# Performance work log

Measured on AMD Instinct MI355X. Metric: run time of the kernel, lower is better.

Reference implementation:

```python
import jax, jax.numpy as jnp
import numpy as np

EPS = 1e-7
N_CAPS1 = 1152  # 32 maps * 6 * 6
D_CAPS1 = 8
N_CAPS2 = 10
D_CAPS2 = 16


def squash(s, axis=-1):
    sq = jnp.sum(jnp.square(s), axis=axis, keepdims=True)
    return (sq / (1.0 + sq)) * s / jnp.sqrt(sq + EPS)


def conv2d_relu(x, w, b, stride):
    y = jax.lax.conv_general_dilated(
        x, w, window_strides=(stride, stride), padding='VALID',
        dimension_numbers=('NHWC', 'HWIO', 'NHWC'))
    return jax.nn.relu(y + b)


def setup_inputs() -> dict:
    key = jax.random.key(0)
    ks = jax.random.split(key, 10)
    B = 128
    image = jax.random.normal(ks[0], (B, 28, 28, 1), dtype=jnp.float32)
    target = jax.random.randint(ks[1], (B,), 0, N_CAPS2)
    conv1_w = jax.random.normal(ks[2], (9, 9, 1, 256), dtype=jnp.float32) * 0.05
    conv1_b = jnp.zeros((256,), jnp.float32)
    conv2_w = jax.random.normal(ks[3], (9, 9, 256, 256), dtype=jnp.float32) * 0.01
    conv2_b = jnp.zeros((256,), jnp.float32)
    W = jax.random.normal(ks[4], (1, N_CAPS1, N_CAPS2, D_CAPS2, D_CAPS1), dtype=jnp.float32) * 0.1
    d1_w = jax.random.normal(ks[5], (N_CAPS2 * D_CAPS2, 512), dtype=jnp.float32) * 0.05
    d1_b = jnp.zeros((512,), jnp.float32)
    d2_w = jax.random.normal(ks[6], (512, 1024), dtype=jnp.float32) * 0.05
    d2_b = jnp.zeros((1024,), jnp.float32)
    do_w = jax.random.normal(ks[7], (1024, 28 * 28), dtype=jnp.float32) * 0.05
    do_b = jnp.zeros((28 * 28,), jnp.float32)
    return dict(image=image, target=target, conv1_w=conv1_w, conv1_b=conv1_b,
                conv2_w=conv2_w, conv2_b=conv2_b, W=W,
                d1_w=d1_w, d1_b=d1_b, d2_w=d2_w, d2_b=d2_b, do_w=do_w, do_b=do_b)


def reference(image, target, conv1_w, conv1_b, conv2_w, conv2_b, W,
              d1_w, d1_b, d2_w, d2_b, do_w, do_b):
    B = image.shape[0]
    # Convolutional feature extraction: 28x28x1 -> 20x20x256 -> 6x6x256
    x = conv2d_relu(image, conv1_w, conv1_b, 1)
    x = conv2d_relu(x, conv2_w, conv2_b, 2)
    # Primary capsules [B, 1152, 8]
    pc = squash(x.reshape(B, N_CAPS1, D_CAPS1), axis=-1)
    # Prediction vectors u_hat[b,i,j,d] (einsum replaces tile+matmul)
    u_hat = jnp.einsum('ijdk,bik->bijd', W[0], pc)[..., None]  # [B,1152,10,16,1]
    # --- dynamic routing, 2 rounds ---
    raw = jnp.zeros((B, N_CAPS1, N_CAPS2, 1, 1), jnp.float32)
    c1 = jax.nn.softmax(raw, axis=2)
    s1 = jnp.sum(c1 * u_hat, axis=1, keepdims=True)      # [B,1,10,16,1]
    v1 = squash(s1, axis=-2)
    uv1 = jnp.sum(u_hat * v1, axis=-2, keepdims=True)    # agreement [B,1152,10,1,1]
    raw = raw + uv1
    c2 = jax.nn.softmax(raw, axis=2)
    s2 = jnp.sum(c2 * u_hat, axis=1, keepdims=True)
    v2 = squash(s2, axis=-2)                              # [B,1,10,16,1]
    norm_v2 = jnp.sqrt(jnp.sum(jnp.square(v2), axis=-2, keepdims=True) + EPS)  # [B,1,10,1,1]
    y_pred = jnp.squeeze(jnp.argmax(norm_v2, axis=2), axis=(1, 2))             # [B,1]
    # training=True path: reconstruction mask from target labels
    mask = jax.nn.one_hot(target, N_CAPS2, dtype=jnp.float32).reshape(-1, 1, N_CAPS2, 1, 1)
    masked = v2 * mask
    # Decoder
    h = masked.reshape(B, -1, N_CAPS2 * D_CAPS2)  # [B,1,160]
    h = jax.nn.relu(h @ d1_w + d1_b)
    h = jax.nn.relu(h @ d2_w + d2_b)
    dec = jax.nn.sigmoid(h @ do_w + do_b)         # [B,1,784]
    return (norm_v2, y_pred, dec)
```

## Files before the change

kernel.cpp:

```cpp
#include <hip/hip_runtime.h>
#include <hip/hip_bf16.h>

#define EPSQ 1e-7f

#define BSZ 128
#define M2 4608
#define K2 20736
#define KSTEPS 648

#define WS_C1H   0
#define WS_C1L   6553600
#define WS_W2TH  13107200
#define WS_W2TL  15761408
#define WS_CPART 18415616
#define WS_PC    0
#define WS_S1P   1179648
#define WS_S2P   4128768
#define WS_V1    7077888
#define WS_H0    7098368
#define WS_NRM   7118848
#define WS_H1    13107200
#define WS_H2    13172736

typedef __attribute__((ext_vector_type(8))) short short8;
typedef __attribute__((ext_vector_type(4))) float floatx4;

#define DOT8(W0, W1, P) ((W0).x*(P)[0] + (W0).y*(P)[1] + (W0).z*(P)[2] + (W0).w*(P)[3] + \
                         (W1).x*(P)[4] + (W1).y*(P)[5] + (W1).z*(P)[6] + (W1).w*(P)[7])

__device__ inline ushort bf16_rne(float x) {
    union { float f; unsigned u; } v; v.f = x;
    unsigned r = v.u + 0x7FFFu + ((v.u >> 16) & 1u);
    return (ushort)(r >> 16);
}
__device__ inline float bf16_to_f(ushort h) {
    union { unsigned u; float f; } v; v.u = ((unsigned)h) << 16;
    return v.f;
}

__global__ __launch_bounds__(256) void convprep_kernel(const float* __restrict__ img,
        const float* __restrict__ w1, const float* __restrict__ b1,
        const float* __restrict__ w2,
        ushort* __restrict__ c1h, ushort* __restrict__ c1l,
        ushort* __restrict__ w2th, ushort* __restrict__ w2tl) {
    __shared__ float sm[4160];
    int t = threadIdx.x;
    int bid = blockIdx.x;
    if (bid < 2560) {
        int b = bid / 20, oh = bid % 20;
        if (t < 252) sm[t] = img[b * 784 + oh * 28 + t];
        __syncthreads();
        float acc[20];
#pragma unroll
        for (int ow = 0; ow < 20; ++ow) acc[ow] = 0.f;
        for (int kh = 0; kh < 9; ++kh) {
            float row[28];
#pragma unroll
            for (int c = 0; c < 28; ++c) row[c] = sm[kh * 28 + c];
#pragma unroll
            for (int kw = 0; kw < 9; ++kw) {
                float wv = w1[(kh * 9 + kw) * 256 + t];
#pragma unroll
                for (int ow = 0; ow < 20; ++ow) acc[ow] += row[kw + ow] * wv;
            }
        }
        float bias = b1[t];
        size_t opos = ((size_t)(b * 20 + oh) * 20) * 256 + t;
#pragma unroll
        for (int ow = 0; ow < 20; ++ow) {
            float x = fmaxf(acc[ow] + bias, 0.f);
            ushort h = bf16_rne(x);
            c1h[opos + (size_t)ow * 256] = h;
            c1l[opos + (size_t)ow * 256] = bf16_rne(x - bf16_to_f(h));
        }
    } else {
        int pb = bid - 2560;
        int kt = pb >> 2, nt = pb & 3;
        int tn = t & 63, t4 = t >> 6;
#pragma unroll
        for (int i = 0; i < 16; ++i) {
            int k = i * 4 + t4;
            sm[k * 65 + tn] = w2[(size_t)(kt * 64 + k) * 256 + nt * 64 + tn];
        }
        __syncthreads();
        int tk = t & 63;
#pragma unroll
        for (int i = 0; i < 16; ++i) {
            int n = i * 4 + t4;
            float x = sm[tk * 65 + n];
            ushort h = bf16_rne(x);
            ushort lo = bf16_rne(x - bf16_to_f(h));
            size_t o = (size_t)(nt * 64 + n) * 20736 + kt * 64 + tk;
            w2th[o] = h; w2tl[o] = lo;
        }
    }
}

#define LDS_AH 0
#define LDS_AL 4096
#define LDS_BH 8192
#define LDS_BL 16384
__global__ __launch_bounds__(256) void conv2_mfma_kernel(
        const ushort* __restrict__ c1h, const ushort* __restrict__ c1l,
        const ushort* __restrict__ w2th, const ushort* __restrict__ w2tl,
        float* __restrict__ part, int nsteps, int nwg) {
    int bid = blockIdx.x;
    int v = (bid & 7) * (nwg >> 3) + (bid >> 3);
    int mt = v % 72, grp = v / 72;
    int nt = grp & 1, ks = grp >> 1;
    int t = threadIdx.x;
    int m0 = mt * 64, n0 = nt * 128;
    __shared__ __attribute__((aligned(16))) ushort lds[24576];

    int sr = t >> 3, sc = t & 7;
    int mA0 = m0 + sr, mA1 = m0 + sr + 32;
    int b0_ = mA0 / 36, r0_ = mA0 % 36;
    int b1_ = mA1 / 36, r1_ = mA1 % 36;
    int pb0 = ((b0_ * 20 + (r0_ / 6) * 2) * 20 + (r0_ % 6) * 2) * 256;
    int pb1 = ((b1_ * 20 + (r1_ / 6) * 2) * 20 + (r1_ % 6) * 2) * 256;
    size_t wb = (size_t)(n0 + sr) * 20736 + sc * 8;
    int wOff = sr * 64 + ((sc ^ (sr & 7)) * 8);

    int lane = t & 63, wave = t >> 6;
    int l15 = lane & 15, g = lane >> 4;
    int wrb = (wave >> 1) * 32, wcb = (wave & 1) * 64;

    floatx4 acc[2][4];
#pragma unroll
    for (int mi = 0; mi < 2; ++mi)
#pragma unroll
        for (int nj = 0; nj < 4; ++nj) acc[mi][nj] = (floatx4)0.f;

    int st0 = ks * nsteps;
    uint4 A0h, A1h, A0l, A1l, B0h, B1h, B2h, B3h, B0l, B1l, B2l, B3l;
#define LOADG64(ST) { \
        int kb = (ST) * 64; \
        int khkw = kb >> 8; int kh = khkw / 9, kw = khkw - kh * 9; \
        int ao = (kh * 20 + kw) * 256 + (kb & 255) + sc * 8; \
        A0h = *(const uint4*)(c1h + pb0 + ao); \
        A1h = *(const uint4*)(c1h + pb1 + ao); \
        A0l = *(const uint4*)(c1l + pb0 + ao); \
        A1l = *(const uint4*)(c1l + pb1 + ao); \
        size_t bo = wb + kb; \
        B0h = *(const uint4*)(w2th + bo); \
        B1h = *(const uint4*)(w2th + bo + (size_t)32 * 20736); \
        B2h = *(const uint4*)(w2th + bo + (size_t)64 * 20736); \
        B3h = *(const uint4*)(w2th + bo + (size_t)96 * 20736); \
        B0l = *(const uint4*)(w2tl + bo); \
        B1l = *(const uint4*)(w2tl + bo + (size_t)32 * 20736); \
        B2l = *(const uint4*)(w2tl + bo + (size_t)64 * 20736); \
        B3l = *(const uint4*)(w2tl + bo + (size_t)96 * 20736); }

    LOADG64(st0);
    for (int st = 0; st < nsteps; ++st) {
        __syncthreads();
        *(uint4*)&lds[LDS_AH + wOff]        = A0h;
        *(uint4*)&lds[LDS_AH + wOff + 2048] = A1h;
        *(uint4*)&lds[LDS_AL + wOff]        = A0l;
        *(uint4*)&lds[LDS_AL + wOff + 2048] = A1l;
        *(uint4*)&lds[LDS_BH + wOff]        = B0h;
        *(uint4*)&lds[LDS_BH + wOff + 2048] = B1h;
        *(uint4*)&lds[LDS_BH + wOff + 4096] = B2h;
        *(uint4*)&lds[LDS_BH + wOff + 6144] = B3h;
        *(uint4*)&lds[LDS_BL + wOff]        = B0l;
        *(uint4*)&lds[LDS_BL + wOff + 2048] = B1l;
        *(uint4*)&lds[LDS_BL + wOff + 4096] = B2l;
        *(uint4*)&lds[LDS_BL + wOff + 6144] = B3l;
        __syncthreads();
        if (st + 1 < nsteps) LOADG64(st0 + st + 1);

#pragma unroll
        for (int kk = 0; kk < 2; ++kk) {
            int sl = kk * 4 + g;
            short8 ah[2], al[2], bh[4], bl[4];
#pragma unroll
            for (int mi = 0; mi < 2; ++mi) {
                int r = wrb + mi * 16 + l15;
                int ro = r * 64 + ((sl ^ (r & 7)) * 8);
                ah[mi] = *(const short8*)&lds[LDS_AH + ro];
                al[mi] = *(const short8*)&lds[LDS_AL + ro];
            }
#pragma unroll
            for (int nj = 0; nj < 4; ++nj) {
                int c = wcb + nj * 16 + l15;
                int co = c * 64 + ((sl ^ (c & 7)) * 8);
                bh[nj] = *(const short8*)&lds[LDS_BH + co];
                bl[nj] = *(const short8*)&lds[LDS_BL + co];
            }
#pragma unroll
            for (int mi = 0; mi < 2; ++mi)
#pragma unroll
                for (int nj = 0; nj < 4; ++nj) {
                    acc[mi][nj] = __builtin_amdgcn_mfma_f32_16x16x32_bf16(ah[mi], bh[nj], acc[mi][nj], 0, 0, 0);
                    acc[mi][nj] = __builtin_amdgcn_mfma_f32_16x16x32_bf16(ah[mi], bl[nj], acc[mi][nj], 0, 0, 0);
                    acc[mi][nj] = __builtin_amdgcn_mfma_f32_16x16x32_bf16(al[mi], bh[nj], acc[mi][nj], 0, 0, 0);
                }
        }
    }
    size_t obase = (size_t)ks * M2 * 256;
#pragma unroll
    for (int mi = 0; mi < 2; ++mi)
#pragma unroll
        for (int nj = 0; nj < 4; ++nj) {
            int col = n0 + wcb + nj * 16 + l15;
            int rowb = m0 + wrb + mi * 16 + (lane >> 4) * 4;
#pragma unroll
            for (int r = 0; r < 4; ++r)
                part[obase + (size_t)(rowb + r) * 256 + col] = acc[mi][nj][r];
        }
}

__global__ __launch_bounds__(256) void squash_pc_kernel(const float* __restrict__ part,
        const float* __restrict__ b2, float* __restrict__ pc, int nsplit) {
    int m = blockIdx.x;
    int n = threadIdx.x;
    size_t idx = (size_t)m * 256 + n;
    const size_t stride = (size_t)M2 * 256;
    float v = 0.f;
    for (int s = 0; s < nsplit; ++s) v += part[idx + s * stride];
    v = fmaxf(v + b2[n], 0.f);
    float sq = v * v;
    sq += __shfl_xor(sq, 1, 8);
    sq += __shfl_xor(sq, 2, 8);
    sq += __shfl_xor(sq, 4, 8);
    float scale = sq / ((1.f + sq) * sqrtf(sq + EPSQ));
    pc[idx] = v * scale;
}

__global__ __launch_bounds__(192) void s1part_kernel(const float* __restrict__ Wm,
        const float* __restrict__ pc, float* __restrict__ s1p) {
    int ic = blockIdx.x, bg = blockIdx.y;
    int i0 = ic * 8, b0 = bg * 16;
    int t = threadIdx.x;
    __shared__ float pcl[16][68];
    for (int e = t; e < 1024; e += 192) {
        int bl = e >> 6, off = e & 63;
        pcl[bl][off] = pc[(size_t)(b0 + bl) * 9216 + i0 * 8 + off];
    }
    __syncthreads();
    if (t >= 160) return;
    float4 w[8][2];
#pragma unroll
    for (int ii = 0; ii < 8; ++ii) {
        const float4* wp = (const float4*)&Wm[(size_t)(i0 + ii) * 1280 + t * 8];
        w[ii][0] = wp[0]; w[ii][1] = wp[1];
    }
    for (int bl = 0; bl < 16; ++bl) {
        float s = 0.f;
#pragma unroll
        for (int ii = 0; ii < 8; ++ii) {
            const float* p = &pcl[bl][ii * 8];
            s += DOT8(w[ii][0], w[ii][1], p);
        }
        s1p[(size_t)ic * 20480 + (b0 + bl) * 160 + t] = s;
    }
}

__global__ __launch_bounds__(256) void v1red_kernel(const float* __restrict__ s1p,
        float* __restrict__ v1) {
    int gid = blockIdx.x * 256 + threadIdx.x;
    float s = 0.f;
    for (int kc = 0; kc < 144; ++kc) s += s1p[(size_t)kc * 20480 + gid];
    s *= 0.1f;
    float sq = s * s;
    sq += __shfl_xor(sq, 1, 16);
    sq += __shfl_xor(sq, 2, 16);
    sq += __shfl_xor(sq, 4, 16);
    sq += __shfl_xor(sq, 8, 16);
    v1[gid] = s * sq / ((1.f + sq) * sqrtf(sq + EPSQ));
}

__global__ __launch_bounds__(192) void c2s2_kernel(const float* __restrict__ Wm,
        const float* __restrict__ pc, const float* __restrict__ v1,
        float* __restrict__ s2p) {
    int ic = blockIdx.x, bg = blockIdx.y;
    int i0 = ic * 8, b0 = bg * 16;
    int t = threadIdx.x;
    __shared__ float pcl[16][68];
    __shared__ float uvl[8][16][10];
    for (int e = t; e < 1024; e += 192) {
        int bl = e >> 6, off = e & 63;
        pcl[bl][off] = pc[(size_t)(b0 + bl) * 9216 + i0 * 8 + off];
    }
    __syncthreads();
    int j = t >> 4;
    float4 w[8][2];
    if (t < 160) {
#pragma unroll
        for (int ii = 0; ii < 8; ++ii) {
            const float4* wp = (const float4*)&Wm[(size_t)(i0 + ii) * 1280 + t * 8];
            w[ii][0] = wp[0]; w[ii][1] = wp[1];
        }
        for (int bl = 0; bl < 16; ++bl) {
            float vv = v1[(b0 + bl) * 160 + t];
#pragma unroll
            for (int ii = 0; ii < 8; ++ii) {
                const float* p = &pcl[bl][ii * 8];
                float u = DOT8(w[ii][0], w[ii][1], p);
                float pr = u * vv;
                pr += __shfl_xor(pr, 1, 16);
                pr += __shfl_xor(pr, 2, 16);
                pr += __shfl_xor(pr, 4, 16);
                pr += __shfl_xor(pr, 8, 16);
                if ((t & 15) == 0) uvl[ii][bl][j] = pr;
            }
        }
    }
    __syncthreads();
    if (t < 128) {
        int ii = t >> 4, bl = t & 15;
        float* uv = uvl[ii][bl];
        float mx = uv[0];
#pragma unroll
        for (int jj = 1; jj < 10; ++jj) mx = fmaxf(mx, uv[jj]);
        float sum = 0.f;
        float ex[10];
#pragma unroll
        for (int jj = 0; jj < 10; ++jj) { ex[jj] = expf(uv[jj] - mx); sum += ex[jj]; }
        float inv = 1.f / sum;
#pragma unroll
        for (int jj = 0; jj < 10; ++jj) uv[jj] = ex[jj] * inv;
    }
    __syncthreads();
    if (t >= 160) return;
    for (int bl = 0; bl < 16; ++bl) {
        float acc = 0.f;
#pragma unroll
        for (int ii = 0; ii < 8; ++ii) {
            const float* p = &pcl[bl][ii * 8];
            float u = DOT8(w[ii][0], w[ii][1], p);
            acc += uvl[ii][bl][j] * u;
        }
        s2p[(size_t)ic * 20480 + (b0 + bl) * 160 + t] = acc;
    }
}

__global__ __launch_bounds__(256) void v2red_kernel(const float* __restrict__ s2p,
        const int* __restrict__ target, float* __restrict__ h0,
        float* __restrict__ nrm, float* __restrict__ out) {
    int gid = blockIdx.x * 256 + threadIdx.x;
    int d = gid & 15, bj = gid >> 4;
    int j = bj % 10, b = bj / 10;
    float s = 0.f;
    for (int kc = 0; kc < 144; ++kc) s += s2p[(size_t)kc * 20480 + gid];
    float sq = s * s;
    sq += __shfl_xor(sq, 1, 16);
    sq += __shfl_xor(sq, 2, 16);
    sq += __shfl_xor(sq, 4, 16);
    sq += __shfl_xor(sq, 8, 16);
    float v = s * sq / ((1.f + sq) * sqrtf(sq + EPSQ));
    float vsq = v * v;
    vsq += __shfl_xor(vsq, 1, 16);
    vsq += __shfl_xor(vsq, 2, 16);
    vsq += __shfl_xor(vsq, 4, 16);
    vsq += __shfl_xor(vsq, 8, 16);
    float norm = sqrtf(vsq + EPSQ);
    h0[gid] = (j == target[b]) ? v : 0.f;
    if (d == 0) { nrm[b * 10 + j] = norm; out[b * 10 + j] = norm; }
}

__global__ __launch_bounds__(256) void fc1_kernel(const float* __restrict__ h0,
        const float* __restrict__ nrm, const float* __restrict__ w,
        const float* __restrict__ bias, float* __restrict__ ypred,
        float* __restrict__ h1) {
    int nc = blockIdx.x, b = blockIdx.y;
    int t = threadIdx.x;
    __shared__ float sk[160];
    if (t < 160) sk[t] = h0[b * 160 + t];
    __syncthreads();
    if (nc == 0 && t == 0) {
        float best = nrm[b * 10]; int am = 0;
#pragma unroll
        for (int jj = 1; jj < 10; ++jj) {
            float n2 = nrm[b * 10 + jj];
            if (n2 > best) { best = n2; am = jj; }
        }
        ypred[b] = (float)am;
    }
    int n = nc * 256 + t;
    float acc = bias[n];
    for (int k = 0; k < 160; ++k) acc += sk[k] * w[k * 512 + n];
    h1[(size_t)b * 512 + n] = fmaxf(acc, 0.f);
}

template <int KDIM, int ACT>
__global__ __launch_bounds__(256) void fc_kernel(const float* __restrict__ in,
        const float* __restrict__ w, const float* __restrict__ bias,
        float* __restrict__ out, int N) {
    int b = blockIdx.y;
    int n = blockIdx.x * 256 + threadIdx.x;
    __shared__ float sk[KDIM];
    for (int r = threadIdx.x; r < KDIM; r += 256) sk[r] = in[(size_t)b * KDIM + r];
    __syncthreads();
    if (n >= N) return;
    float acc = bias[n];
    for (int k = 0; k < KDIM; ++k) acc += sk[k] * w[(size_t)k * N + n];
    if (ACT == 0) acc = fmaxf(acc, 0.f);
    else acc = 1.f / (1.f + expf(-acc));
    out[(size_t)b * N + n] = acc;
}

extern "C" void kernel_launch(void* const* d_in, const int* in_sizes, int n_in,
                              void* d_out, int out_size, void* d_ws, size_t ws_size,
                              hipStream_t stream) {
    const float* image = (const float*)d_in[0];
    const int*   target = (const int*)d_in[1];
    const float* w1  = (const float*)d_in[2];
    const float* b1  = (const float*)d_in[3];
    const float* w2  = (const float*)d_in[4];
    const float* b2  = (const float*)d_in[5];
    const float* Wm  = (const float*)d_in[6];
    const float* d1w = (const float*)d_in[7];
    const float* d1b = (const float*)d_in[8];
    const float* d2w = (const float*)d_in[9];
    const float* d2b = (const float*)d_in[10];
    const float* dow = (const float*)d_in[11];
    const float* dob = (const float*)d_in[12];
    float* out = (float*)d_out;
    float* ws  = (float*)d_ws;

    ushort* c1h  = (ushort*)(ws + WS_C1H);
    ushort* c1l  = (ushort*)(ws + WS_C1L);
    ushort* w2th = (ushort*)(ws + WS_W2TH);
    ushort* w2tl = (ushort*)(ws + WS_W2TL);

    int ksplit = 4;
    if (ws_size >= (size_t)(18415616 + 18 * 1179648) * 4) ksplit = 18;
    else if (ws_size >= (size_t)(18415616 + 12 * 1179648) * 4) ksplit = 12;
    else if (ws_size >= (size_t)(18415616 + 6 * 1179648) * 4) ksplit = 6;
    int nsteps = KSTEPS / ksplit / 2;
    int nwg = 144 * ksplit;

    convprep_kernel<<<3856, 256, 0, stream>>>(image, w1, b1, w2, c1h, c1l, w2th, w2tl);
    conv2_mfma_kernel<<<nwg, 256, 0, stream>>>(c1h, c1l, w2th, w2tl,
                                               ws + WS_CPART, nsteps, nwg);
    squash_pc_kernel<<<4608, 256, 0, stream>>>(ws + WS_CPART, b2, ws + WS_PC, ksplit);
    s1part_kernel<<<dim3(144, 8), 192, 0, stream>>>(Wm, ws + WS_PC, ws + WS_S1P);
    v1red_kernel<<<80, 256, 0, stream>>>(ws + WS_S1P, ws + WS_V1);
    c2s2_kernel<<<dim3(144, 8), 192, 0, stream>>>(Wm, ws + WS_PC, ws + WS_V1, ws + WS_S2P);
    v2red_kernel<<<80, 256, 0, stream>>>(ws + WS_S2P, target, ws + WS_H0,
                                         ws + WS_NRM, out);
    fc1_kernel<<<dim3(2, 128), 256, 0, stream>>>(ws + WS_H0, ws + WS_NRM,
                                                 d1w, d1b, out + 1280, ws + WS_H1);
    fc_kernel<512, 0><<<dim3(4, 128), 256, 0, stream>>>(ws + WS_H1, d2w, d2b, ws + WS_H2, 1024);
    fc_kernel<1024, 1><<<dim3(4, 128), 256, 0, stream>>>(ws + WS_H2, dow, dob, out + 1408, 784);
}
```

Baseline: 501.8 us.

## Replace routing partial-sum buffers with atomics and stage conv2 output through LDS

The two routing reduction kernels (v1red, v2red) are removed. The s1 and s2 partial sums are now accumulated with atomicAdd into small buffers that squash_pc zeroes. The squash steps are folded into c2s2 and fc1, and the conv2 MFMA epilogue stages its tile through LDS so it can write coalesced float4 rows. This cuts two launches and the large partial-buffer writes and reads, at the cost of atomic contention and nondeterministic summation order.

```diff
diff --git a/kernel.cpp b/kernel.cpp
--- a/kernel.cpp
+++ b/kernel.cpp
@@ -14,11 +14,7 @@
 #define WS_W2TL  15761408
 #define WS_CPART 18415616
 #define WS_PC    0
-#define WS_S1P   1179648
-#define WS_S2P   4128768
-#define WS_V1    7077888
-#define WS_H0    7098368
-#define WS_NRM   7118848
+#define WS_S12A  1179648
 #define WS_H1    13107200
 #define WS_H2    13172736
 
@@ -197,23 +193,35 @@
                 }
         }
     }
+    __syncthreads();
+    float* ldsf = (float*)lds;
+#pragma unroll
+    for (int mi = 0; mi < 2; ++mi)
+#pragma unroll
+        for (int nj = 0; nj < 4; ++nj) {
+            int col = wcb + nj * 16 + l15;
+            int rw = wrb + mi * 16 + (lane >> 4) * 4;
+#pragma unroll
+            for (int r = 0; r < 4; ++r)
+                ldsf[(rw + r) * 132 + col] = acc[mi][nj][r];
+        }
+    __syncthreads();
     size_t obase = (size_t)ks * M2 * 256;
 #pragma unroll
-    for (int mi = 0; mi < 2; ++mi)
-#pragma unroll
-        for (int nj = 0; nj < 4; ++nj) {
-            int col = n0 + wcb + nj * 16 + l15;
-            int rowb = m0 + wrb + mi * 16 + (lane >> 4) * 4;
-#pragma unroll
-            for (int r = 0; r < 4; ++r)
-                part[obase + (size_t)(rowb + r) * 256 + col] = acc[mi][nj][r];
-        }
+    for (int i = 0; i < 8; ++i) {
+        int f = i * 256 + t;
+        int row = f >> 5, c4 = f & 31;
+        float4 val = *(const float4*)&ldsf[row * 132 + c4 * 4];
+        *(float4*)&part[obase + (size_t)(m0 + row) * 256 + n0 + c4 * 4] = val;
+    }
 }
 
 __global__ __launch_bounds__(256) void squash_pc_kernel(const float* __restrict__ part,
-        const float* __restrict__ b2, float* __restrict__ pc, int nsplit) {
+        const float* __restrict__ b2, float* __restrict__ pc,
+        float* __restrict__ s12acc, int nsplit) {
     int m = blockIdx.x;
     int n = threadIdx.x;
+    if (m < 160) s12acc[m * 256 + n] = 0.f;
     size_t idx = (size_t)m * 256 + n;
     const size_t stride = (size_t)M2 * 256;
     float v = 0.f;
@@ -228,7 +236,7 @@
 }
 
 __global__ __launch_bounds__(192) void s1part_kernel(const float* __restrict__ Wm,
-        const float* __restrict__ pc, float* __restrict__ s1p) {
+        const float* __restrict__ pc, float* __restrict__ s1acc) {
     int ic = blockIdx.x, bg = blockIdx.y;
     int i0 = ic * 8, b0 = bg * 16;
     int t = threadIdx.x;
@@ -252,27 +260,13 @@
             const float* p = &pcl[bl][ii * 8];
             s += DOT8(w[ii][0], w[ii][1], p);
         }
-        s1p[(size_t)ic * 20480 + (b0 + bl) * 160 + t] = s;
-    }
-}
-
-__global__ __launch_bounds__(256) void v1red_kernel(const float* __restrict__ s1p,
-        float* __restrict__ v1) {
-    int gid = blockIdx.x * 256 + threadIdx.x;
-    float s = 0.f;
-    for (int kc = 0; kc < 144; ++kc) s += s1p[(size_t)kc * 20480 + gid];
-    s *= 0.1f;
-    float sq = s * s;
-    sq += __shfl_xor(sq, 1, 16);
-    sq += __shfl_xor(sq, 2, 16);
-    sq += __shfl_xor(sq, 4, 16);
-    sq += __shfl_xor(sq, 8, 16);
-    v1[gid] = s * sq / ((1.f + sq) * sqrtf(sq + EPSQ));
+        atomicAdd(&s1acc[(b0 + bl) * 160 + t], s);
+    }
 }
 
 __global__ __launch_bounds__(192) void c2s2_kernel(const float* __restrict__ Wm,
-        const float* __restrict__ pc, const float* __restrict__ v1,
-        float* __restrict__ s2p) {
+        const float* __restrict__ pc, const float* __restrict__ s1acc,
+        float* __restrict__ s2acc) {
     int ic = blockIdx.x, bg = blockIdx.y;
     int i0 = ic * 8, b0 = bg * 16;
     int t = threadIdx.x;
@@ -292,7 +286,13 @@
             w[ii][0] = wp[0]; w[ii][1] = wp[1];
         }
         for (int bl = 0; bl < 16; ++bl) {
-            float vv = v1[(b0 + bl) * 160 + t];
+            float s1v = s1acc[(b0 + bl) * 160 + t] * 0.1f;
+            float q = s1v * s1v;
+            q += __shfl_xor(q, 1, 16);
+            q += __shfl_xor(q, 2, 16);
+            q += __shfl_xor(q, 4, 16);
+            q += __shfl_xor(q, 8, 16);
+            float vv = s1v * q / ((1.f + q) * sqrtf(q + EPSQ));
 #pragma unroll
             for (int ii = 0; ii < 8; ++ii) {
                 const float* p = &pcl[bl][ii * 8];
@@ -331,51 +331,45 @@
             float u = DOT8(w[ii][0], w[ii][1], p);
             acc += uvl[ii][bl][j] * u;
         }
-        s2p[(size_t)ic * 20480 + (b0 + bl) * 160 + t] = acc;
-    }
-}
-
-__global__ __launch_bounds__(256) void v2red_kernel(const float* __restrict__ s2p,
-        const int* __restrict__ target, float* __restrict__ h0,
-        float* __restrict__ nrm, float* __restrict__ out) {
-    int gid = blockIdx.x * 256 + threadIdx.x;
-    int d = gid & 15, bj = gid >> 4;
-    int j = bj % 10, b = bj / 10;
-    float s = 0.f;
-    for (int kc = 0; kc < 144; ++kc) s += s2p[(size_t)kc * 20480 + gid];
-    float sq = s * s;
-    sq += __shfl_xor(sq, 1, 16);
-    sq += __shfl_xor(sq, 2, 16);
-    sq += __shfl_xor(sq, 4, 16);
-    sq += __shfl_xor(sq, 8, 16);
-    float v = s * sq / ((1.f + sq) * sqrtf(sq + EPSQ));
-    float vsq = v * v;
-    vsq += __shfl_xor(vsq, 1, 16);
-    vsq += __shfl_xor(vsq, 2, 16);
-    vsq += __shfl_xor(vsq, 4, 16);
-    vsq += __shfl_xor(vsq, 8, 16);
-    float norm = sqrtf(vsq + EPSQ);
-    h0[gid] = (j == target[b]) ? v : 0.f;
-    if (d == 0) { nrm[b * 10 + j] = norm; out[b * 10 + j] = norm; }
-}
-
-__global__ __launch_bounds__(256) void fc1_kernel(const float* __restrict__ h0,
-        const float* __restrict__ nrm, const float* __restrict__ w,
-        const float* __restrict__ bias, float* __restrict__ ypred,
+        atomicAdd(&s2acc[(b0 + bl) * 160 + t], acc);
+    }
+}
+
+__global__ __launch_bounds__(256) void fc1_kernel(const float* __restrict__ s2acc,
+        const int* __restrict__ target, const float* __restrict__ w,
+        const float* __restrict__ bias, float* __restrict__ out,
         float* __restrict__ h1) {
     int nc = blockIdx.x, b = blockIdx.y;
     int t = threadIdx.x;
     __shared__ float sk[160];
-    if (t < 160) sk[t] = h0[b * 160 + t];
+    __shared__ float nl[10];
+    if (t < 160) {
+        float s = s2acc[b * 160 + t];
+        float sq = s * s;
+        sq += __shfl_xor(sq, 1, 16);
+        sq += __shfl_xor(sq, 2, 16);
+        sq += __shfl_xor(sq, 4, 16);
+        sq += __shfl_xor(sq, 8, 16);
+        float v = s * sq / ((1.f + sq) * sqrtf(sq + EPSQ));
+        float vsq = v * v;
+        vsq += __shfl_xor(vsq, 1, 16);
+        vsq += __shfl_xor(vsq, 2, 16);
+        vsq += __shfl_xor(vsq, 4, 16);
+        vsq += __shfl_xor(vsq, 8, 16);
+        float norm = sqrtf(vsq + EPSQ);
+        int j = t >> 4;
+        sk[t] = (j == target[b]) ? v : 0.f;
+        if ((t & 15) == 0) {
+            nl[j] = norm;
+            if (nc == 0) out[b * 10 + j] = norm;
+        }
+    }
     __syncthreads();
     if (nc == 0 && t == 0) {
-        float best = nrm[b * 10]; int am = 0;
-#pragma unroll
-        for (int jj = 1; jj < 10; ++jj) {
-            float n2 = nrm[b * 10 + jj];
-            if (n2 > best) { best = n2; am = jj; }
-        }
-        ypred[b] = (float)am;
+        float best = nl[0]; int am = 0;
+#pragma unroll
+        for (int jj = 1; jj < 10; ++jj) if (nl[jj] > best) { best = nl[jj]; am = jj; }
+        out[1280 + b] = (float)am;
     }
     int n = nc * 256 + t;
     float acc = bias[n];
@@ -431,17 +425,18 @@
     int nsteps = KSTEPS / ksplit / 2;
     int nwg = 144 * ksplit;
 
+    float* s1acc = ws + WS_S12A;
+    float* s2acc = ws + WS_S12A + 20480;
+
     convprep_kernel<<<3856, 256, 0, stream>>>(image, w1, b1, w2, c1h, c1l, w2th, w2tl);
     conv2_mfma_kernel<<<nwg, 256, 0, stream>>>(c1h, c1l, w2th, w2tl,
                                                ws + WS_CPART, nsteps, nwg);
-    squash_pc_kernel<<<4608, 256, 0, stream>>>(ws + WS_CPART, b2, ws + WS_PC, ksplit);
-    s1part_kernel<<<dim3(144, 8), 192, 0, stream>>>(Wm, ws + WS_PC, ws + WS_S1P);
-    v1red_kernel<<<80, 256, 0, stream>>>(ws + WS_S1P, ws + WS_V1);
-    c2s2_kernel<<<dim3(144, 8), 192, 0, stream>>>(Wm, ws + WS_PC, ws + WS_V1, ws + WS_S2P);
-    v2red_kernel<<<80, 256, 0, stream>>>(ws + WS_S2P, target, ws + WS_H0,
-                                         ws + WS_NRM, out);
-    fc1_kernel<<<dim3(2, 128), 256, 0, stream>>>(ws + WS_H0, ws + WS_NRM,
-                                                 d1w, d1b, out + 1280, ws + WS_H1);
+    squash_pc_kernel<<<4608, 256, 0, stream>>>(ws + WS_CPART, b2, ws + WS_PC,
+                                               ws + WS_S12A, ksplit);
+    s1part_kernel<<<dim3(144, 8), 192, 0, stream>>>(Wm, ws + WS_PC, s1acc);
+    c2s2_kernel<<<dim3(144, 8), 192, 0, stream>>>(Wm, ws + WS_PC, s1acc, s2acc);
+    fc1_kernel<<<dim3(2, 128), 256, 0, stream>>>(s2acc, target, d1w, d1b,
+                                                 out, ws + WS_H1);
     fc_kernel<512, 0><<<dim3(4, 128), 256, 0, stream>>>(ws + WS_H1, d2w, d2b, ws + WS_H2, 1024);
     fc_kernel<1024, 1><<<dim3(4, 128), 256, 0, stream>>>(ws + WS_H2, dow, dob, out + 1408, 784);
 }
```

New measurement: 425.0 us. 1.18x faster.
